# Optimization experiments

Measured on AMD Instinct MI355X. Metric: run time of the kernel, lower is better.

Reference implementation:

```python
import jax, jax.numpy as jnp
import numpy as np

N_P, N_W, F_IN = 512, 3584, 256
H1, O1 = 8, 32
H2, O2 = 8, 256
BATCH = 1024
NEG_SLOPE = 0.2


def _xavier(key, shape):
    fan_in, fan_out = shape[-2], shape[-1]
    lim = jnp.sqrt(6.0 / (fan_in + fan_out))
    return jax.random.uniform(key, shape, jnp.float32, -lim, lim)


def setup_inputs() -> dict:
    key = jax.random.key(0)
    ks = jax.random.split(key, 16)
    return {
        "input": jax.random.uniform(ks[0], (BATCH, N_W), jnp.float32),
        "pern_feature": jax.random.normal(ks[1], (N_P, F_IN), jnp.float32),
        "word_feature": jax.random.normal(ks[2], (N_W, F_IN), jnp.float32),
        "w1": _xavier(ks[3], (H1, F_IN, O1)),
        "a_src1": _xavier(ks[4], (H1, O1, 1)),
        "a_dst1": _xavier(ks[5], (H1, O1, 1)),
        "b1": jnp.zeros((O1,), jnp.float32),
        "w2": _xavier(ks[6], (H2, F_IN, O2)),
        "a_src2": _xavier(ks[7], (H2, F_IN, 1)),
        "a_dst2": _xavier(ks[8], (H2, F_IN, 1)),
        "b2": jnp.zeros((O2,), jnp.float32),
        "W_fc": _xavier(ks[9], (O2, 5)),
        "b_fc": jnp.zeros((5,), jnp.float32),
        "pern_adj": jax.random.randint(ks[10], (N_P, N_P), 0, 2, jnp.int32),
        "word_pern_adj": jax.random.randint(ks[11], (N_P + N_W, N_P + N_W), 0, 2, jnp.int32),
    }


def gat(h, adj, w, a_src, a_dst, bias):
    # h: [N, f_in], adj: [N, N] int, w: [H, f_in, f_out]
    h_prime = jnp.einsum('nf,hfo->hno', h, w)          # [H, N, O]
    t = jnp.tanh(h_prime)
    s_src = jnp.einsum('hno,hoi->hn', t, a_src)        # [H, N]
    s_dst = jnp.einsum('hno,hoi->hn', t, a_dst)        # [H, N]
    attn = s_src[:, :, None] + s_dst[:, None, :]       # [H, N, N]
    attn = jnp.where(attn >= 0, attn, NEG_SLOPE * attn)  # leaky_relu
    attn = jnp.where(adj[None, :, :] > 0, attn, -jnp.inf)
    attn = jax.nn.softmax(attn, axis=-1)
    out = jnp.einsum('hnm,hmo->hno', attn, h_prime)    # [H, N, O]
    return out + bias


def reference(input, pern_feature, word_feature, w1, a_src1, a_dst1, b1,
              w2, a_src2, a_dst2, b2, W_fc, b_fc, pern_adj, word_pern_adj):
    n_p = pern_feature.shape[0]
    # GAT 1 over personality graph
    h1 = gat(pern_feature, pern_adj, w1, a_src1, a_dst1, b1)       # [H1, n_p, O1]
    hiddn_pp = jnp.transpose(h1, (1, 0, 2)).reshape(n_p, -1)        # [n_p, H1*O1]
    hiddn_pp = jax.nn.elu(hiddn_pp)
    # dropout is identity in eval mode
    hiddn_wp = jnp.concatenate([word_feature, hiddn_pp], axis=0)    # [N, 256]
    h2 = gat(hiddn_wp, word_pern_adj, w2, a_src2, a_dst2, b2)       # [H2, N, O2]
    hiddn_wp2 = h2.mean(axis=0)                                     # [N, O2]
    hiddn_w = hiddn_wp2[:word_feature.shape[0], :]                  # [n_w, O2]
    x = (input @ hiddn_w) / input.sum(axis=1, keepdims=True)        # [B, O2]
    return x @ W_fc + b_fc                                          # [B, 5]
```

## Files before the change

kernel.cpp:

```cpp
#include <hip/hip_runtime.h>
#include <hip/hip_bf16.h>
#include <math.h>

#define NP 512
#define NW 3584
#define NT 4096
#define FIN 256
#define H1 8
#define O1 32
#define H2 8
#define O2 256
#define NEG 0.2f

typedef __attribute__((ext_vector_type(8))) short bf16x8;
typedef __attribute__((ext_vector_type(4))) float f32x4;
typedef __attribute__((ext_vector_type(2))) float v2f;
typedef unsigned long long u64;

__device__ __forceinline__ unsigned short f2bf(float f) {
    unsigned u = __float_as_uint(f);
    unsigned r = (u + 0x7FFF + ((u >> 16) & 1)) >> 16;
    return (unsigned short)r;
}

__device__ __forceinline__ float fast_tanh(float x) {
    float ex = __expf(2.0f * x);
    return 1.0f - 2.0f / (ex + 1.0f);
}

__global__ __launch_bounds__(256) void k_prep(
    const float* __restrict__ wf, const float* __restrict__ pf,
    const float* __restrict__ w1, const float* __restrict__ a_src1,
    const float* __restrict__ a_dst1, const float* __restrict__ w2,
    const float* __restrict__ b2, const float* __restrict__ W_fc,
    const int* __restrict__ wp_adj,
    unsigned short* __restrict__ abf, unsigned short* __restrict__ btbf,
    float* __restrict__ hp1, float* __restrict__ ss1, float* __restrict__ sd1,
    u64* __restrict__ packed, float* __restrict__ cvec)
{
    __shared__ float feat[2][FIN];
    __shared__ float red[4][5];
    int blk = blockIdx.x;
    int t = threadIdx.x;
    if (blk < 3584) {
        int i = blk * 256 + t;
        abf[i] = f2bf(wf[i]);
    } else if (blk < 3840) {
        int n0 = (blk - 3584) * 2;
        feat[0][t] = pf[n0 * FIN + t];
        feat[1][t] = pf[(n0 + 1) * FIN + t];
        __syncthreads();
        int h = t >> 5, o = t & 31;
        float acc0 = 0.f, acc1 = 0.f;
        const float* wcol = w1 + h * FIN * O1 + o;
        #pragma unroll 4
        for (int f = 0; f < FIN; f++) {
            float w = wcol[f * O1];
            acc0 += feat[0][f] * w;
            acc1 += feat[1][f] * w;
        }
        hp1[n0 * 256 + t] = acc0;
        hp1[(n0 + 1) * 256 + t] = acc1;
        float as = a_src1[h * O1 + o];
        float ad = a_dst1[h * O1 + o];
        float accs[2] = {acc0, acc1};
        #pragma unroll
        for (int i = 0; i < 2; i++) {
            float th = tanhf(accs[i]);
            float vs = th * as, vd = th * ad;
            #pragma unroll
            for (int off = 1; off < 32; off <<= 1) {
                vs += __shfl_xor(vs, off);
                vd += __shfl_xor(vd, off);
            }
            if (o == 0) { ss1[h * NP + n0 + i] = vs; sd1[h * NP + n0 + i] = vd; }
        }
    } else if (blk < 5888) {
        int idx = (blk - 3840) * 256 + t;
        int f = idx & 255, o = (idx >> 8) & 255, h = idx >> 16;
        btbf[idx] = f2bf(w2[(h * FIN + f) * O2 + o]);
    } else if (blk < 6784) {
        int w = t >> 6, l = t & 63;
        int r = (blk - 5888) * 4 + w;
        const int4* row = (const int4*)(wp_adj + (size_t)r * NT);
        for (int c4 = 0; c4 < 16; c4++) {
            int4 x = row[c4 * 64 + l];
            u64 nib = (u64)((x.x != 0 ? 1 : 0) | (x.y != 0 ? 2 : 0) |
                            (x.z != 0 ? 4 : 0) | (x.w != 0 ? 8 : 0));
            u64 v = nib << (4 * (l & 15));
            v |= __shfl_xor(v, 1);
            v |= __shfl_xor(v, 2);
            v |= __shfl_xor(v, 4);
            v |= __shfl_xor(v, 8);
            if ((l & 15) == 0) packed[(size_t)r * 64 + c4 * 4 + (l >> 4)] = v;
        }
    } else {
        float v[5];
        #pragma unroll
        for (int j = 0; j < 5; j++) v[j] = b2[t] * W_fc[t * 5 + j];
        #pragma unroll
        for (int off = 1; off < 64; off <<= 1)
            #pragma unroll
            for (int j = 0; j < 5; j++) v[j] += __shfl_xor(v[j], off);
        int w = t >> 6, l = t & 63;
        if (l == 0) { for (int j = 0; j < 5; j++) red[w][j] = v[j]; }
        __syncthreads();
        if (t == 0)
            for (int j = 0; j < 5; j++) cvec[j] = red[0][j] + red[1][j] + red[2][j] + red[3][j];
    }
}

__global__ __launch_bounds__(256) void k_gat1_attn(
    const int* __restrict__ adj, const float* __restrict__ hp1,
    const float* __restrict__ ss1, const float* __restrict__ sd1,
    const float* __restrict__ b1, unsigned short* __restrict__ abf)
{
    __shared__ float p[2][H1][NP];
    __shared__ float den[2][H1];
    int t = threadIdx.x;
    int n0 = blockIdx.x * 2;
    for (int rr = 0; rr < 32; rr++) {
        int idx = rr * 256 + t;
        int i = idx >> 12, h = (idx >> 9) & 7, m = idx & 511;
        float a = adj[(n0 + i) * NP + m] > 0 ? 1.0f : 0.0f;
        float e = ss1[h * NP + n0 + i] + sd1[h * NP + m];
        e = fmaxf(e, NEG * e);
        p[i][h][m] = a * __expf(e);
    }
    __syncthreads();
    int w = t >> 6, l = t & 63;
    {
        int i = w & 1;
        #pragma unroll
        for (int hh = 0; hh < 4; hh++) {
            int h = (w >> 1) * 4 + hh;
            float s = 0;
            #pragma unroll
            for (int q = 0; q < 8; q++) s += p[i][h][l + 64 * q];
            #pragma unroll
            for (int off = 1; off < 64; off <<= 1) s += __shfl_xor(s, off);
            if (l == 0) den[i][h] = s;
        }
    }
    __syncthreads();
    int h = t >> 5, o = t & 31;
    float acc[2] = {0, 0};
    #pragma unroll 4
    for (int m = 0; m < NP; m++) {
        float v = hp1[m * 256 + t];
        acc[0] += p[0][h][m] * v;
        acc[1] += p[1][h][m] * v;
    }
    float bo = b1[o];
    #pragma unroll
    for (int i = 0; i < 2; i++) {
        float r = acc[i] / den[i][h] + bo;
        r = r > 0.f ? r : expm1f(r);
        abf[(NW + n0 + i) * FIN + t] = f2bf(r);
    }
}

__global__ __launch_bounds__(256) void k_gemm_hp2(
    const unsigned short* __restrict__ abf, const unsigned short* __restrict__ btbf,
    const float* __restrict__ a_src2, const float* __restrict__ a_dst2,
    const float* __restrict__ W_fc, float* __restrict__ gpart)
{
    int bid = blockIdx.x;
    int h = bid >> 6;
    int rem = bid & 63;
    int mt = rem >> 1, nt = rem & 1;
    int w = threadIdx.x >> 6, l = threadIdx.x & 63;
    int m0 = mt * 128 + (w >> 1) * 64;
    int n0 = nt * 128 + (w & 1) * 64;
    int lr = l & 15, lq = l >> 4;
    const unsigned short* bbase = btbf + h * O2 * FIN;
    f32x4 acc[4][4];
    #pragma unroll
    for (int i = 0; i < 4; i++)
        #pragma unroll
        for (int j = 0; j < 4; j++) acc[i][j] = (f32x4){0.f, 0.f, 0.f, 0.f};
    for (int k = 0; k < FIN; k += 32) {
        bf16x8 a[4], b[4];
        int kc = k + lq * 8;
        #pragma unroll
        for (int i = 0; i < 4; i++)
            a[i] = *(const bf16x8*)(abf + (m0 + i * 16 + lr) * FIN + kc);
        #pragma unroll
        for (int j = 0; j < 4; j++)
            b[j] = *(const bf16x8*)(bbase + (n0 + j * 16 + lr) * FIN + kc);
        #pragma unroll
        for (int i = 0; i < 4; i++)
            #pragma unroll
            for (int j = 0; j < 4; j++)
                acc[i][j] = __builtin_amdgcn_mfma_f32_16x16x32_bf16(a[i], b[j], acc[i][j], 0, 0, 0);
    }
    int slice = nt * 2 + (w & 1);
    float as[4], ad[4], wfc[4][5];
    #pragma unroll
    for (int j = 0; j < 4; j++) {
        int col = n0 + j * 16 + lr;
        as[j] = a_src2[h * O2 + col];
        ad[j] = a_dst2[h * O2 + col];
        #pragma unroll
        for (int jj = 0; jj < 5; jj++) wfc[j][jj] = W_fc[col * 5 + jj];
    }
    float* base = gpart + ((size_t)h * 4 + slice) * NT * 8;
    #pragma unroll
    for (int i = 0; i < 4; i++) {
        #pragma unroll
        for (int r = 0; r < 4; r++) {
            float s[7] = {0,0,0,0,0,0,0};
            #pragma unroll
            for (int j = 0; j < 4; j++) {
                float x = acc[i][j][r];
                float th = fast_tanh(x);
                s[0] += th * as[j];
                s[1] += th * ad[j];
                #pragma unroll
                for (int jj = 0; jj < 5; jj++) s[2 + jj] += x * wfc[j][jj];
            }
            #pragma unroll
            for (int off = 1; off < 16; off <<= 1)
                #pragma unroll
                for (int q = 0; q < 7; q++) s[q] += __shfl_xor(s[q], off);
            if (lr == 0) {
                int m = m0 + i * 16 + lq * 4 + r;
                float* dst = base + (size_t)m * 8;
                #pragma unroll
                for (int q = 0; q < 7; q++) dst[q] = s[q];
            }
        }
    }
}

__global__ __launch_bounds__(256) void k_comb_hp2(
    const float* __restrict__ gpart,
    float* __restrict__ Etab, float* __restrict__ Eptab, float* __restrict__ T)
{
    int idx = blockIdx.x * 256 + threadIdx.x;
    float s[7] = {0,0,0,0,0,0,0};
    #pragma unroll
    for (int sl = 0; sl < 4; sl++) {
        const float* p = gpart + (((size_t)(idx >> 12) * 4 + sl) * NT + (idx & (NT - 1))) * 8;
        #pragma unroll
        for (int q = 0; q < 7; q++) s[q] += p[q];
    }
    Etab[idx]  = __expf(s[0]);
    Eptab[idx] = __expf(NEG * s[0]);
    float4 t0 = {__expf(s[1]), __expf(NEG * s[1]), 1.0f, s[2]};
    float4 t1 = {s[3], s[4], s[5], s[6]};
    *(float4*)(T + (size_t)idx * 8)     = t0;
    *(float4*)(T + (size_t)idx * 8 + 4) = t1;
}

__global__ __launch_bounds__(512) void k_gat2_attn(
    const u64* __restrict__ packed, const float* __restrict__ Etab,
    const float* __restrict__ Eptab, const float* __restrict__ T,
    float* __restrict__ part)
{
    __shared__ unsigned pw[64 * 64];
    int t = threadIdx.x;
    int w = t >> 6, l = t & 63;
    int b = blockIdx.x;
    int nb = b % 56;
    int h  = (b / 56) & 7;
    int c  = b / 448;
    int rbase = nb * 64;
    const unsigned* p32 = (const unsigned*)packed;
    #pragma unroll
    for (int u = 0; u < 8; u++) {
        int idx = u * 512 + t;
        int row = idx >> 6, word = idx & 63;
        pw[idx] = p32[(size_t)(rbase + row) * 128 + c * 64 + word];
    }
    __syncthreads();
    int n0 = rbase + w * 8;
    u64 epk[8];
    #pragma unroll
    for (int i = 0; i < 8; i++) {
        int r = h * NT + n0 + i;
        unsigned e  = __builtin_amdgcn_readfirstlane(__float_as_uint(Etab[r]));
        unsigned ep = __builtin_amdgcn_readfirstlane(__float_as_uint(Eptab[r]));
        epk[i] = ((u64)ep << 32) | e;
    }
    v2f accA[8], accB[8], accC[8];
    #pragma unroll
    for (int i = 0; i < 8; i++) {
        accA[i] = (v2f){0.f, 0.f}; accB[i] = (v2f){0.f, 0.f}; accC[i] = (v2f){0.f, 0.f};
    }
    const float* Th = T + ((size_t)h * NT + c * 2048) * 8;
    const unsigned* wbase = pw + w * 512 + (l >> 5);
    int lsh = l & 31;
    for (int q = 0; q < 32; q++) {
        const float* tp = Th + (size_t)(q * 64 + l) * 8;
        f32x4 t0 = *(const f32x4*)tp;
        f32x4 t1 = *(const f32x4*)(tp + 4);
        v2f ffp = {t0.x, t0.y};
        v2f g01 = {t0.z, t0.w};
        v2f g12 = {t1.x, t1.y};
        v2f g34 = {t1.z, t1.w};
        #pragma unroll
        for (int i = 0; i < 8; i++) {
            unsigned word = wbase[i * 64 + q * 2];
            float bm = (float)((word >> lsh) & 1u);
            v2f pab;
            asm("v_pk_mul_f32 %0, %1, %2" : "=v"(pab) : "v"(ffp), "s"(epk[i]));
            float pp = fmaxf(pab.x, pab.y) * bm;
            v2f ppv; ppv.x = pp; ppv.y = pp;
            asm("v_pk_fma_f32 %0, %1, %2, %0" : "+v"(accA[i]) : "v"(ppv), "v"(g01));
            asm("v_pk_fma_f32 %0, %1, %2, %0" : "+v"(accB[i]) : "v"(ppv), "v"(g12));
            asm("v_pk_fma_f32 %0, %1, %2, %0" : "+v"(accC[i]) : "v"(ppv), "v"(g34));
        }
    }
    #pragma unroll
    for (int i = 0; i < 8; i++) {
        float v[6];
        v[0] = accA[i].x; v[1] = accA[i].y;
        v[2] = accB[i].x; v[3] = accB[i].y;
        v[4] = accC[i].x; v[5] = accC[i].y;
        #pragma unroll
        for (int off = 1; off < 64; off <<= 1)
            #pragma unroll
            for (int k = 0; k < 6; k++) v[k] += __shfl_xor(v[k], off);
        if (l == 0) {
            float* dst = part + (((size_t)c * NW + n0 + i) * 8 + h) * 6;
            #pragma unroll
            for (int k = 0; k < 6; k++) dst[k] = v[k];
        }
    }
}

__global__ __launch_bounds__(256) void k_gat2_comb(const float* __restrict__ part,
                                                   float* __restrict__ hf) {
    int idx = blockIdx.x * 256 + threadIdx.x;
    int n = idx >> 3, h = idx & 7;
    float den = 0, num[5] = {0,0,0,0,0};
    #pragma unroll
    for (int cc = 0; cc < 2; cc++) {
        const float* p = part + (((size_t)cc * NW + n) * 8 + h) * 6;
        den += p[0];
        #pragma unroll
        for (int j = 0; j < 5; j++) num[j] += p[1 + j];
    }
    float inv = 1.0f / (den * 8.0f);
    float v[5];
    #pragma unroll
    for (int j = 0; j < 5; j++) v[j] = num[j] * inv;
    #pragma unroll
    for (int off = 1; off < 8; off <<= 1)
        #pragma unroll
        for (int j = 0; j < 5; j++) v[j] += __shfl_xor(v[j], off);
    if (h == 0) {
        #pragma unroll
        for (int j = 0; j < 5; j++) hf[n * 5 + j] = v[j];
    }
}

__global__ __launch_bounds__(256) void k_final(
    const float* __restrict__ input, const float* __restrict__ hf,
    const float* __restrict__ cvec, const float* __restrict__ b_fc,
    float* __restrict__ out)
{
    int b = blockIdx.x, t = threadIdx.x;
    const float4* row4 = (const float4*)(input + (size_t)b * NW);
    const float4* hf4 = (const float4*)hf;
    float s = 0.f, a[5] = {0.f, 0.f, 0.f, 0.f, 0.f};
    for (int idx = t; idx < NW / 4; idx += 256) {
        float4 x = row4[idx];
        float f[20];
        #pragma unroll
        for (int q = 0; q < 5; q++) *(float4*)(f + 4 * q) = hf4[idx * 5 + q];
        s += x.x + x.y + x.z + x.w;
        #pragma unroll
        for (int j = 0; j < 5; j++)
            a[j] += x.x * f[j] + x.y * f[5 + j] + x.z * f[10 + j] + x.w * f[15 + j];
    }
    #pragma unroll
    for (int off = 1; off < 64; off <<= 1) {
        s += __shfl_xor(s, off);
        #pragma unroll
        for (int j = 0; j < 5; j++) a[j] += __shfl_xor(a[j], off);
    }
    __shared__ float red[4][6];
    int w = t >> 6, l = t & 63;
    if (l == 0) { red[w][0] = s; for (int j = 0; j < 5; j++) red[w][j + 1] = a[j]; }
    __syncthreads();
    if (t < 5) {
        float st = red[0][0] + red[1][0] + red[2][0] + red[3][0];
        float aj = red[0][t + 1] + red[1][t + 1] + red[2][t + 1] + red[3][t + 1];
        out[b * 5 + t] = aj / st + cvec[t] + b_fc[t];
    }
}

extern "C" void kernel_launch(void* const* d_in, const int* in_sizes, int n_in,
                              void* d_out, int out_size, void* d_ws, size_t ws_size,
                              hipStream_t stream) {
    const float* input   = (const float*)d_in[0];
    const float* pf      = (const float*)d_in[1];
    const float* wf      = (const float*)d_in[2];
    const float* w1      = (const float*)d_in[3];
    const float* a_src1  = (const float*)d_in[4];
    const float* a_dst1  = (const float*)d_in[5];
    const float* b1      = (const float*)d_in[6];
    const float* w2      = (const float*)d_in[7];
    const float* a_src2  = (const float*)d_in[8];
    const float* a_dst2  = (const float*)d_in[9];
    const float* b2      = (const float*)d_in[10];
    const float* W_fc    = (const float*)d_in[11];
    const float* b_fc    = (const float*)d_in[12];
    const int* pern_adj  = (const int*)d_in[13];
    const int* wp_adj    = (const int*)d_in[14];
    float* out = (float*)d_out;

    char* ws = (char*)d_ws;
    unsigned short* abf    = (unsigned short*)(ws);
    unsigned short* btbf   = (unsigned short*)(ws + 2097152);
    float*          hp1    = (float*)(ws + 3145728);
    float*          ss1    = (float*)(ws + 3670016);
    float*          sd1    = (float*)(ws + 3686400);
    float*          Etab   = (float*)(ws + 3833856);
    float*          Eptab  = (float*)(ws + 3964928);
    float*          T      = (float*)(ws + 4096000);
    float*          hf     = (float*)(ws + 5144576);
    float*          cvec   = (float*)(ws + 5216256);
    u64*            packed = (u64*)(ws + 5216512);
    float*          gpart  = (float*)(ws + 7051520);
    float*          part   = (float*)(ws + 11245824);

    k_prep<<<6785, 256, 0, stream>>>(wf, pf, w1, a_src1, a_dst1, w2, b2, W_fc,
                                     wp_adj, abf, btbf, hp1, ss1, sd1, packed, cvec);
    k_gat1_attn<<<256, 256, 0, stream>>>(pern_adj, hp1, ss1, sd1, b1, abf);
    k_gemm_hp2<<<512, 256, 0, stream>>>(abf, btbf, a_src2, a_dst2, W_fc, gpart);
    k_comb_hp2<<<128, 256, 0, stream>>>(gpart, Etab, Eptab, T);
    k_gat2_attn<<<896, 512, 0, stream>>>(packed, Etab, Eptab, T, part);
    k_gat2_comb<<<112, 256, 0, stream>>>(part, hf);
    k_final<<<1024, 256, 0, stream>>>(input, hf, cvec, b_fc, out);
}
```

Before: 283.2 us.

## Transpose adjacency bitmask, vectorize prep conversions, shorten attention reductions

The adjacency bitmask is now stored word-major (transposed), so each wave in the GAT2 attention kernel reads its eight row masks with two 128-bit LDS loads instead of eight scalar loads. The final cross-lane reduction in that kernel stops at 8 lanes and writes 8 partial sums per row, which the combine kernel then adds. The prep kernel converts word features with float4 loads and transposes w2 through an LDS tile for coalesced access. It also adds a launch-bounds occupancy hint. In exchange, the partial buffer grows larger and the mask writes in prep become strided.

```diff
diff --git a/kernel.cpp b/kernel.cpp
--- a/kernel.cpp
+++ b/kernel.cpp
@@ -36,17 +36,21 @@
     const int* __restrict__ wp_adj,
     unsigned short* __restrict__ abf, unsigned short* __restrict__ btbf,
     float* __restrict__ hp1, float* __restrict__ ss1, float* __restrict__ sd1,
-    u64* __restrict__ packed, float* __restrict__ cvec)
-{
+    unsigned* __restrict__ maskT, float* __restrict__ cvec)
+{
+    __shared__ float tile[64][65];
     __shared__ float feat[2][FIN];
     __shared__ float red[4][5];
     int blk = blockIdx.x;
     int t = threadIdx.x;
-    if (blk < 3584) {
-        int i = blk * 256 + t;
-        abf[i] = f2bf(wf[i]);
-    } else if (blk < 3840) {
-        int n0 = (blk - 3584) * 2;
+    if (blk < 896) {
+        int idx4 = blk * 256 + t;
+        float4 x = ((const float4*)wf)[idx4];
+        ushort4 y;
+        y.x = f2bf(x.x); y.y = f2bf(x.y); y.z = f2bf(x.z); y.w = f2bf(x.w);
+        ((ushort4*)abf)[idx4] = y;
+    } else if (blk < 1152) {
+        int n0 = (blk - 896) * 2;
         feat[0][t] = pf[n0 * FIN + t];
         feat[1][t] = pf[(n0 + 1) * FIN + t];
         __syncthreads();
@@ -75,13 +79,27 @@
             }
             if (o == 0) { ss1[h * NP + n0 + i] = vs; sd1[h * NP + n0 + i] = vd; }
         }
-    } else if (blk < 5888) {
-        int idx = (blk - 3840) * 256 + t;
-        int f = idx & 255, o = (idx >> 8) & 255, h = idx >> 16;
-        btbf[idx] = f2bf(w2[(h * FIN + f) * O2 + o]);
-    } else if (blk < 6784) {
+    } else if (blk < 1280) {
+        int blk2 = blk - 1152;
+        int h = blk2 >> 4;
+        int f0 = ((blk2 >> 2) & 3) * 64;
+        int o0 = (blk2 & 3) * 64;
+        #pragma unroll
+        for (int rr = 0; rr < 16; rr++) {
+            int f = rr * 4 + (t >> 6);
+            int o = t & 63;
+            tile[f][o] = w2[((size_t)(h * FIN + f0 + f)) * O2 + o0 + o];
+        }
+        __syncthreads();
+        #pragma unroll
+        for (int rr = 0; rr < 16; rr++) {
+            int o = rr * 4 + (t >> 6);
+            int f = t & 63;
+            btbf[((size_t)(h * O2 + o0 + o)) * FIN + f0 + f] = f2bf(tile[f][o]);
+        }
+    } else if (blk < 2176) {
         int w = t >> 6, l = t & 63;
-        int r = (blk - 5888) * 4 + w;
+        int r = (blk - 1280) * 4 + w;
         const int4* row = (const int4*)(wp_adj + (size_t)r * NT);
         for (int c4 = 0; c4 < 16; c4++) {
             int4 x = row[c4 * 64 + l];
@@ -92,7 +110,11 @@
             v |= __shfl_xor(v, 2);
             v |= __shfl_xor(v, 4);
             v |= __shfl_xor(v, 8);
-            if ((l & 15) == 0) packed[(size_t)r * 64 + c4 * 4 + (l >> 4)] = v;
+            if ((l & 15) == 0) {
+                int qw = c4 * 4 + (l >> 4);
+                maskT[(size_t)(2 * qw) * NW + r]     = (unsigned)v;
+                maskT[(size_t)(2 * qw + 1) * NW + r] = (unsigned)(v >> 32);
+            }
         }
     } else {
         float v[5];
@@ -253,8 +275,8 @@
     *(float4*)(T + (size_t)idx * 8 + 4) = t1;
 }
 
-__global__ __launch_bounds__(512) void k_gat2_attn(
-    const u64* __restrict__ packed, const float* __restrict__ Etab,
+__global__ __launch_bounds__(512, 4) void k_gat2_attn(
+    const unsigned* __restrict__ maskT, const float* __restrict__ Etab,
     const float* __restrict__ Eptab, const float* __restrict__ T,
     float* __restrict__ part)
 {
@@ -266,12 +288,11 @@
     int h  = (b / 56) & 7;
     int c  = b / 448;
     int rbase = nb * 64;
-    const unsigned* p32 = (const unsigned*)packed;
     #pragma unroll
     for (int u = 0; u < 8; u++) {
         int idx = u * 512 + t;
-        int row = idx >> 6, word = idx & 63;
-        pw[idx] = p32[(size_t)(rbase + row) * 128 + c * 64 + word];
+        int wd = idx >> 6, row = idx & 63;
+        pw[idx] = maskT[(size_t)(c * 64 + wd) * NW + rbase + row];
     }
     __syncthreads();
     int n0 = rbase + w * 8;
@@ -289,7 +310,7 @@
         accA[i] = (v2f){0.f, 0.f}; accB[i] = (v2f){0.f, 0.f}; accC[i] = (v2f){0.f, 0.f};
     }
     const float* Th = T + ((size_t)h * NT + c * 2048) * 8;
-    const unsigned* wbase = pw + w * 512 + (l >> 5);
+    const unsigned* mbase = pw + (l >> 5) * 64 + w * 8;
     int lsh = l & 31;
     for (int q = 0; q < 32; q++) {
         const float* tp = Th + (size_t)(q * 64 + l) * 8;
@@ -299,10 +320,12 @@
         v2f g01 = {t0.z, t0.w};
         v2f g12 = {t1.x, t1.y};
         v2f g34 = {t1.z, t1.w};
+        uint4 ma = *(const uint4*)(mbase + q * 128);
+        uint4 mb = *(const uint4*)(mbase + q * 128 + 4);
+        unsigned wv[8] = {ma.x, ma.y, ma.z, ma.w, mb.x, mb.y, mb.z, mb.w};
         #pragma unroll
         for (int i = 0; i < 8; i++) {
-            unsigned word = wbase[i * 64 + q * 2];
-            float bm = (float)((word >> lsh) & 1u);
+            float bm = (float)((wv[i] >> lsh) & 1u);
             v2f pab;
             asm("v_pk_mul_f32 %0, %1, %2" : "=v"(pab) : "v"(ffp), "s"(epk[i]));
             float pp = fmaxf(pab.x, pab.y) * bm;
@@ -319,11 +342,11 @@
         v[2] = accB[i].x; v[3] = accB[i].y;
         v[4] = accC[i].x; v[5] = accC[i].y;
         #pragma unroll
-        for (int off = 1; off < 64; off <<= 1)
+        for (int off = 1; off < 8; off <<= 1)
             #pragma unroll
             for (int k = 0; k < 6; k++) v[k] += __shfl_xor(v[k], off);
-        if (l == 0) {
-            float* dst = part + (((size_t)c * NW + n0 + i) * 8 + h) * 6;
+        if ((l & 7) == 0) {
+            float* dst = part + ((((size_t)c * NW + n0 + i) * 8 + h) * 8 + (l >> 3)) * 8;
             #pragma unroll
             for (int k = 0; k < 6; k++) dst[k] = v[k];
         }
@@ -337,10 +360,15 @@
     float den = 0, num[5] = {0,0,0,0,0};
     #pragma unroll
     for (int cc = 0; cc < 2; cc++) {
-        const float* p = part + (((size_t)cc * NW + n) * 8 + h) * 6;
-        den += p[0];
-        #pragma unroll
-        for (int j = 0; j < 5; j++) num[j] += p[1 + j];
+        #pragma unroll
+        for (int s = 0; s < 8; s++) {
+            const float* p = part + ((((size_t)cc * NW + n) * 8 + h) * 8 + s) * 8;
+            float4 a = *(const float4*)p;
+            float4 bq = *(const float4*)(p + 4);
+            den += a.x;
+            num[0] += a.y; num[1] += a.z; num[2] += a.w;
+            num[3] += bq.x; num[4] += bq.y;
+        }
     }
     float inv = 1.0f / (den * 8.0f);
     float v[5];
@@ -423,16 +451,16 @@
     float*          T      = (float*)(ws + 4096000);
     float*          hf     = (float*)(ws + 5144576);
     float*          cvec   = (float*)(ws + 5216256);
-    u64*            packed = (u64*)(ws + 5216512);
+    unsigned*       maskT  = (unsigned*)(ws + 5216512);
     float*          gpart  = (float*)(ws + 7051520);
     float*          part   = (float*)(ws + 11245824);
 
-    k_prep<<<6785, 256, 0, stream>>>(wf, pf, w1, a_src1, a_dst1, w2, b2, W_fc,
-                                     wp_adj, abf, btbf, hp1, ss1, sd1, packed, cvec);
+    k_prep<<<2177, 256, 0, stream>>>(wf, pf, w1, a_src1, a_dst1, w2, b2, W_fc,
+                                     wp_adj, abf, btbf, hp1, ss1, sd1, maskT, cvec);
     k_gat1_attn<<<256, 256, 0, stream>>>(pern_adj, hp1, ss1, sd1, b1, abf);
     k_gemm_hp2<<<512, 256, 0, stream>>>(abf, btbf, a_src2, a_dst2, W_fc, gpart);
     k_comb_hp2<<<128, 256, 0, stream>>>(gpart, Etab, Eptab, T);
-    k_gat2_attn<<<896, 512, 0, stream>>>(packed, Etab, Eptab, T, part);
+    k_gat2_attn<<<896, 512, 0, stream>>>(maskT, Etab, Eptab, T, part);
     k_gat2_comb<<<112, 256, 0, stream>>>(part, hf);
     k_final<<<1024, 256, 0, stream>>>(input, hf, cvec, b_fc, out);
 }
```

After: 281.9 us. Within noise of the previous version (-0.5%).
